# Optimization experiments

Measured on AMD Instinct MI355X. Metric: run time of the kernel, lower is better.

Reference implementation:

```python
import jax, jax.numpy as jnp
import numpy as np

EPS = 1e-12      # F.normalize eps
BN_EPS = 1e-5    # BatchNorm1d eps


def _l2norm(x):
    # x: (B, E, S); normalize over channel dim E (torch F.normalize default dim=1)
    n = jnp.sqrt(jnp.sum(x * x, axis=1, keepdims=True))
    return x / jnp.maximum(n, EPS)


def _conv1x1(w, b, x):
    # 1x1 Conv1d: w (O, E), b (O,), x (B, S, E) -> (B, O, S)
    return jnp.einsum('oe,bse->bos', w, x) + b[None, :, None]


def _batchnorm(x, g, b):
    # train-mode BatchNorm1d on (B, F): biased batch stats over dim 0
    m = jnp.mean(x, axis=0)
    v = jnp.var(x, axis=0)
    return (x - m) * jax.lax.rsqrt(v + BN_EPS) * g + b


def _pairwise(X, Y, wx, bx, wy, by, g, be, mxw, mxb, myw, myb):
    # X: (B, Sx, e), Y: (B, Sy, e)
    Xn = _l2norm(_conv1x1(wx, bx, X))           # (B, E, Sx)
    Yn = _l2norm(_conv1x1(wy, by, Y))           # (B, E, Sy)
    S = jnp.einsum('bex,bey->bxy', Xn, Yn)       # (B, Sx, Sy)
    B, Sx, Sy = S.shape
    S = _batchnorm(S.reshape(B, Sx * Sy), g, be).reshape(B, Sx, Sy)
    potX = jnp.einsum('y,bxy->bx', mxw, S) + mxb  # margin_X: Conv1d(Sy,1,1)
    potY = jnp.einsum('x,bxy->by', myw, S) + myb  # margin_Y: Conv1d(Sx,1,1)
    return potX, potY


def _pairwise_self(X, wx, bx, wy, by, g, be, mxw, mxb):
    # Pairwise with Y=None: embed_X and embed_Y both applied to X; only X_poten returned
    Xn = _l2norm(_conv1x1(wx, bx, X))
    Yn = _l2norm(_conv1x1(wy, by, X))
    S = jnp.einsum('bex,bey->bxy', Xn, Yn)
    B, Sx, Sy = S.shape
    S = _batchnorm(S.reshape(B, Sx * Sy), g, be).reshape(B, Sx, Sy)
    return jnp.einsum('y,bxy->bx', mxw, S) + mxb


def _unary(X, w1, b1, w2, b2):
    # Unary: conv1d e->e, relu, (dropout=identity in eval), conv1d e->1
    h = jax.nn.relu(_conv1x1(w1, b1, X))         # (B, E, S)
    return jnp.einsum('e,bes->bs', w2, h) + b2


def _forward(utils, un_w1, un_b1, un_w2, un_b2,
             sp_wx, sp_bx, sp_wy, sp_by, sp_g, sp_b, sp_mxw, sp_mxb,
             pw_wx, pw_bx, pw_wy, pw_by, pw_g, pw_b, pw_mxw, pw_mxb, pw_myw, pw_myb,
             red_w):
    # utils: (3, B, S, e)
    unp = jax.vmap(_unary)(utils, un_w1, un_b1, un_w2, un_b2)                    # (3, B, S)
    sfp = jax.vmap(_pairwise_self)(utils, sp_wx, sp_bx, sp_wy, sp_by,
                                   sp_g, sp_b, sp_mxw, sp_mxb)                   # (3, B, S)
    # pairwise pairs in combinations order: (0,1), (0,2), (1,2)
    idx_i = jnp.array([0, 0, 1])
    idx_j = jnp.array([1, 2, 2])
    pX, pY = jax.vmap(_pairwise)(utils[idx_i], utils[idx_j],
                                 pw_wx, pw_bx, pw_wy, pw_by, pw_g, pw_b,
                                 pw_mxw, pw_mxb, pw_myw, pw_myb)                 # (3, B, S) each
    pots = [
        [unp[0], sfp[0], pX[0], pX[1]],   # util 0: ij of (0,1), ij of (0,2)
        [unp[1], sfp[1], pY[0], pX[2]],   # util 1: ji of (0,1), ij of (1,2)
        [unp[2], sfp[2], pY[1], pY[2]],   # util 2: ji of (0,2), ji of (1,2)
    ]
    outs = []
    for i in range(3):
        P = jnp.stack(pots[i], axis=1)                 # (B, 4, S)
        red = jnp.einsum('k,bks->bs', red_w[i], P)     # Conv1d(4,1,1,bias=False)
        attn = jax.nn.softmax(red, axis=1)             # softmax over spatial dim
        outs.append(jnp.einsum('bse,bs->be', utils[i], attn))  # bmm(utils^T, attn)
    return jnp.stack(outs, axis=0)                     # (3, B, e)


def setup_inputs() -> dict:
    key = jax.random.key(0)
    ks = iter(jax.random.split(key, 32))
    def rn(shape, scale=0.05):
        return jax.random.normal(next(ks), shape, dtype=jnp.float32) * scale
    e, S, B, NU, NP = 128, 1024, 32, 3, 3
    F = S * S
    return dict(
        utils=rn((NU, B, S, e), 1.0),
        un_w1=rn((NU, e, e)), un_b1=rn((NU, e)), un_w2=rn((NU, e)), un_b2=rn((NU,)),
        sp_wx=rn((NU, e, e)), sp_bx=rn((NU, e)), sp_wy=rn((NU, e, e)), sp_by=rn((NU, e)),
        sp_g=jnp.ones((NU, F), jnp.float32), sp_b=jnp.zeros((NU, F), jnp.float32),
        sp_mxw=rn((NU, S)), sp_mxb=rn((NU,)),
        pw_wx=rn((NP, e, e)), pw_bx=rn((NP, e)), pw_wy=rn((NP, e, e)), pw_by=rn((NP, e)),
        pw_g=jnp.ones((NP, F), jnp.float32), pw_b=jnp.zeros((NP, F), jnp.float32),
        pw_mxw=rn((NP, S)), pw_mxb=rn((NP,)), pw_myw=rn((NP, S)), pw_myb=rn((NP,)),
        red_w=rn((NU, 4)),
    )


def reference(utils, un_w1, un_b1, un_w2, un_b2,
              sp_wx, sp_bx, sp_wy, sp_by, sp_g, sp_b, sp_mxw, sp_mxb,
              pw_wx, pw_bx, pw_wy, pw_by, pw_g, pw_b, pw_mxw, pw_mxb, pw_myw, pw_myb,
              red_w):
    return _forward(utils, un_w1, un_b1, un_w2, un_b2,
                    sp_wx, sp_bx, sp_wy, sp_by, sp_g, sp_b, sp_mxw, sp_mxb,
                    pw_wx, pw_bx, pw_wy, pw_by, pw_g, pw_b, pw_mxw, pw_mxb, pw_myw, pw_myb,
                    red_w)
```

## Files before the change

### kernel.cpp

```cpp
#include <hip/hip_runtime.h>
#include <math.h>

constexpr int EE = 128;
constexpr int NS = 1024;
constexpr int NB = 32;
constexpr size_t BSE = (size_t)NB * NS * EE;

typedef __attribute__((ext_vector_type(4))) float f32x4;
typedef __attribute__((ext_vector_type(8))) short s16x8;
typedef __attribute__((ext_vector_type(4))) short s16x4;
typedef __attribute__((ext_vector_type(8))) __bf16 bf16v8;

__device__ __forceinline__ f32x4 mfma16(s16x8 a, s16x8 b, f32x4 c) {
  return __builtin_amdgcn_mfma_f32_16x16x32_bf16(
      __builtin_bit_cast(bf16v8, a), __builtin_bit_cast(bf16v8, b), c, 0, 0, 0);
}

__device__ __forceinline__ unsigned short f2bf(float f) {
  unsigned u = __builtin_bit_cast(unsigned, f);
  u += 0x7FFFu + ((u >> 16) & 1u);
  return (unsigned short)(u >> 16);
}
__device__ __forceinline__ float bf2f(unsigned short h) {
  unsigned u = ((unsigned)h) << 16;
  return __builtin_bit_cast(float, u);
}

__device__ __forceinline__ int swz(int b)  { return b ^ (((b >> 8) & 7) << 4); }
__device__ __forceinline__ int swz7(int b) { return b ^ (((b >> 7) & 7) << 4); }

__device__ __forceinline__ void gl_lds16(const void* gptr, void* lptr) {
  auto g = (const __attribute__((address_space(1))) unsigned int*)gptr;
  auto l = (__attribute__((address_space(3))) unsigned int*)lptr;
  __builtin_amdgcn_global_load_lds(g, l, 16, 0, 0);
}

__device__ __forceinline__ void stage32k(const char* gsrc, char* ldst, int wv, int lane) {
#pragma unroll
  for (int c = 0; c < 8; ++c) {
    int uoff = c*4096 + wv*1024;
    gl_lds16(gsrc + swz(uoff + lane*16), ldst + uoff);
  }
}

__device__ __forceinline__ void stage_half(const char* tile, char* ldst, int kh, int wv, int lane) {
#pragma unroll
  for (int c = 0; c < 4; ++c) {
    int uoff = c*4096 + wv*1024;
    int sa = swz7(uoff + lane*16);
    gl_lds16(tile + (sa >> 7)*256 + kh*128 + (sa & 127), ldst + uoff);
  }
}

constexpr size_t EMB_OFF   = 0;
constexpr size_t UNP_OFF   = EMB_OFF + 12ull * BSE * 2;
constexpr size_t RB_OFF    = UNP_OFF + 3ull * NB * NS * 4;
constexpr size_t CX_OFF    = RB_OFF + 6ull * NS * NS * 2;
constexpr size_t POTX_OFF  = CX_OFF + 6ull * NS * 4;
constexpr size_t PYP_OFF   = POTX_OFF + 6ull * NB * NS * 4;
constexpr size_t CY_OFF    = PYP_OFF + 3ull * NB * 8 * NS * 4;
constexpr size_t CXP_OFF   = CY_OFF + 6ull * NS * 4;
constexpr size_t CYP_OFF   = CXP_OFF + 6ull * 8 * NS * 4;

__global__ __launch_bounds__(256, 2) void embed_kernel(
    const float* __restrict__ utils,
    const float* __restrict__ un_w1, const float* __restrict__ un_b1,
    const float* __restrict__ un_w2, const float* __restrict__ un_b2,
    const float* __restrict__ sp_wx, const float* __restrict__ sp_bx,
    const float* __restrict__ sp_wy, const float* __restrict__ sp_by,
    const float* __restrict__ pw_wx, const float* __restrict__ pw_bx,
    const float* __restrict__ pw_wy, const float* __restrict__ pw_by,
    unsigned short* __restrict__ emb, float* __restrict__ unp)
{
  const int u  = blockIdx.x >> 9;
  const int pt = blockIdx.x & 511;

  __shared__ short lA[64*128];
  __shared__ short lB[128*128];
  __shared__ float redbuf[64];

  const int t = threadIdx.x;
  {
    const char* src = (const char*)(utils + (size_t)u*BSE + (size_t)pt*64*EE);
#pragma unroll
    for (int c = 0; c < 8; ++c) {
      int off = c*4096 + t*16;
      float4 v = *(const float4*)(src + off);
      s16x4 h;
      h.x = (short)f2bf(v.x); h.y = (short)f2bf(v.y);
      h.z = (short)f2bf(v.z); h.w = (short)f2bf(v.w);
      *(s16x4*)((char*)lA + swz(off >> 1)) = h;
    }
  }

  const int lane = t & 63, wv = t >> 6;
  const int wrE = wv & 1, wcE = wv >> 1;
  const int cL = lane & 15, r4 = (lane >> 4) * 4, k8 = (lane >> 4) * 8;

  for (int m = 0; m < 5; ++m) {
    const float* W; const float* bias;
    unsigned short* dst = nullptr;
    int mode;
    if (m == 0)      { W = un_w1 + u*EE*EE; bias = un_b1 + u*EE; mode = 0; }
    else if (m == 1) { W = sp_wx + u*EE*EE; bias = sp_bx + u*EE; dst = emb + (size_t)(2*u)*BSE;   mode = 1; }
    else if (m == 2) { W = sp_wy + u*EE*EE; bias = sp_by + u*EE; dst = emb + (size_t)(2*u+1)*BSE; mode = 1; }
    else {
      int q, side;
      if (u == 0)      { q = (m == 3) ? 0 : 1; side = 0; }
      else if (u == 1) { if (m == 3) { q = 0; side = 1; } else { q = 2; side = 0; } }
      else             { q = (m == 3) ? 1 : 2; side = 1; }
      W    = (side == 0 ? pw_wx : pw_wy) + q*EE*EE;
      bias = (side == 0 ? pw_bx : pw_by) + q*EE;
      dst  = emb + (size_t)(2*(3+q)+side)*BSE;
      mode = 1;
    }

    __syncthreads();
    {
      const char* wsrc = (const char*)W;
#pragma unroll
      for (int c = 0; c < 16; ++c) {
        int off = c*4096 + t*16;
        float4 v = *(const float4*)(wsrc + off);
        s16x4 h;
        h.x = (short)f2bf(v.x); h.y = (short)f2bf(v.y);
        h.z = (short)f2bf(v.z); h.w = (short)f2bf(v.w);
        *(s16x4*)((char*)lB + swz(off >> 1)) = h;
      }
    }
    __syncthreads();

    f32x4 acc[2][4];
#pragma unroll
    for (int i = 0; i < 2; ++i)
#pragma unroll
      for (int j = 0; j < 4; ++j) acc[i][j] = f32x4{0.f, 0.f, 0.f, 0.f};

#pragma unroll
    for (int kk = 0; kk < 4; ++kk) {
      s16x8 av[2], bv[4];
#pragma unroll
      for (int i = 0; i < 2; ++i) {
        int row = wrE*32 + i*16 + cL;
        av[i] = *(const s16x8*)((const char*)lA + swz(row*256 + kk*64 + k8*2));
      }
#pragma unroll
      for (int j = 0; j < 4; ++j) {
        int row = wcE*64 + j*16 + cL;
        bv[j] = *(const s16x8*)((const char*)lB + swz(row*256 + kk*64 + k8*2));
      }
#pragma unroll
      for (int i = 0; i < 2; ++i)
#pragma unroll
        for (int j = 0; j < 4; ++j)
          acc[i][j] = mfma16(av[i], bv[j], acc[i][j]);
    }

    if (mode == 0) {
      const float* w2 = un_w2 + u*EE;
      float s[2][4];
#pragma unroll
      for (int i = 0; i < 2; ++i)
#pragma unroll
        for (int r = 0; r < 4; ++r) s[i][r] = 0.f;
#pragma unroll
      for (int i = 0; i < 2; ++i) {
#pragma unroll
        for (int j = 0; j < 4; ++j) {
          int o = wcE*64 + j*16 + cL;
          float bv2 = bias[o], w2v = w2[o];
#pragma unroll
          for (int r = 0; r < 4; ++r) {
            float v = acc[i][j][r] + bv2;
            v = v > 0.f ? v : 0.f;
            s[i][r] += v * w2v;
          }
        }
      }
#pragma unroll
      for (int msk = 1; msk < 16; msk <<= 1)
#pragma unroll
        for (int i = 0; i < 2; ++i)
#pragma unroll
          for (int r = 0; r < 4; ++r)
            s[i][r] += __shfl_xor(s[i][r], msk, 64);
      if (t < 64) redbuf[t] = 0.f;
      __syncthreads();
      if (cL == 0) {
#pragma unroll
        for (int i = 0; i < 2; ++i)
#pragma unroll
          for (int r = 0; r < 4; ++r)
            atomicAdd(&redbuf[wrE*32 + i*16 + r4 + r], s[i][r]);
      }
      __syncthreads();
      if (t < 64) unp[(size_t)u*NB*NS + (size_t)pt*64 + t] = redbuf[t] + un_b2[u];
    } else {
      float nrm[2][4];
#pragma unroll
      for (int i = 0; i < 2; ++i)
#pragma unroll
        for (int r = 0; r < 4; ++r) nrm[i][r] = 0.f;
#pragma unroll
      for (int i = 0; i < 2; ++i) {
#pragma unroll
        for (int j = 0; j < 4; ++j) {
          int o = wcE*64 + j*16 + cL;
          float bv2 = bias[o];
#pragma unroll
          for (int r = 0; r < 4; ++r) {
            acc[i][j][r] += bv2;
            nrm[i][r] += acc[i][j][r] * acc[i][j][r];
          }
        }
      }
#pragma unroll
      for (int msk = 1; msk < 16; msk <<= 1)
#pragma unroll
        for (int i = 0; i < 2; ++i)
#pragma unroll
          for (int r = 0; r < 4; ++r)
            nrm[i][r] += __shfl_xor(nrm[i][r], msk, 64);
      if (t < 64) redbuf[t] = 0.f;
      __syncthreads();
      if (cL == 0) {
#pragma unroll
        for (int i = 0; i < 2; ++i)
#pragma unroll
          for (int r = 0; r < 4; ++r)
            atomicAdd(&redbuf[wrE*32 + i*16 + r4 + r], nrm[i][r]);
      }
      __syncthreads();
#pragma unroll
      for (int i = 0; i < 2; ++i) {
#pragma unroll
        for (int r = 0; r < 4; ++r) {
          float n = redbuf[wrE*32 + i*16 + r4 + r];
          float sc = 1.f / fmaxf(sqrtf(n), 1e-12f);
          size_t pbase = ((size_t)pt*64 + wrE*32 + i*16 + r4 + r) * EE;
#pragma unroll
          for (int j = 0; j < 4; ++j) {
            int o = wcE*64 + j*16 + cL;
            dst[pbase + o] = f2bf(acc[i][j][r] * sc);
          }
        }
      }
    }
  }
}

__global__ __launch_bounds__(256, 2) void pass1_kernel(
    const unsigned short* __restrict__ emb,
    const float* __restrict__ sp_g, const float* __restrict__ sp_b,
    const float* __restrict__ sp_mxw,
    const float* __restrict__ pw_g, const float* __restrict__ pw_b,
    const float* __restrict__ pw_mxw, const float* __restrict__ pw_myw,
    unsigned short* __restrict__ Rb, float* __restrict__ cXpart,
    float* __restrict__ cYpart)
{
  const int bid = blockIdx.x;
  const int p = bid >> 6, xt = (bid >> 3) & 7, yt = bid & 7;
  const char* Xe = (const char*)(emb + (size_t)(2*p)*BSE + (size_t)xt*128*EE);
  const char* Ye = (const char*)(emb + (size_t)(2*p+1)*BSE + (size_t)yt*128*EE);
  __shared__ char lds[65536];
  __shared__ float cxbuf[128];
  __shared__ float cybuf[128];
  const int t = threadIdx.x, lane = t & 63, wv = t >> 6;
  const int wr = wv >> 1, wc = wv & 1, cL = lane & 15, r4 = (lane >> 4) * 4;
  const int q16 = (lane >> 4) * 16;

  f32x4 sS[4][4], sQ[4][4], acc[4][4];
#pragma unroll
  for (int i = 0; i < 4; ++i)
#pragma unroll
    for (int j = 0; j < 4; ++j) { sS[i][j] = f32x4{0.f,0.f,0.f,0.f}; sQ[i][j] = f32x4{0.f,0.f,0.f,0.f}; }

  stage_half(Xe, lds, 0, wv, lane);
  stage_half(Ye, lds + 16384, 0, wv, lane);
  if (t < 128) { cxbuf[t] = 0.f; cybuf[t] = 0.f; }
  __syncthreads();

  for (int s = 0; s < 2*NB; ++s) {
    const int cur = s & 1;
    const char* buf = lds + cur * 32768;
    if (s + 1 < 2*NB) {
      const int b1 = (s + 1) >> 1, kh1 = (s + 1) & 1;
      char* nb = lds + (cur ^ 1) * 32768;
      stage_half(Xe + (size_t)b1*NS*EE*2, nb, kh1, wv, lane);
      stage_half(Ye + (size_t)b1*NS*EE*2, nb + 16384, kh1, wv, lane);
    }
    if ((s & 1) == 0) {
#pragma unroll
      for (int i = 0; i < 4; ++i)
#pragma unroll
        for (int j = 0; j < 4; ++j) acc[i][j] = f32x4{0.f,0.f,0.f,0.f};
    }
#pragma unroll
    for (int kk2 = 0; kk2 < 2; ++kk2) {
      s16x8 av[4], bv[4];
#pragma unroll
      for (int i = 0; i < 4; ++i) {
        int row = wr*64 + i*16 + cL;
        av[i] = *(const s16x8*)(buf + swz7(row*128 + kk2*64 + q16));
      }
#pragma unroll
      for (int j = 0; j < 4; ++j) {
        int row = wc*64 + j*16 + cL;
        bv[j] = *(const s16x8*)(buf + 16384 + swz7(row*128 + kk2*64 + q16));
      }
#pragma unroll
      for (int i = 0; i < 4; ++i)
#pragma unroll
        for (int j = 0; j < 4; ++j)
          acc[i][j] = mfma16(av[i], bv[j], acc[i][j]);
    }
    if (s & 1) {
#pragma unroll
      for (int i = 0; i < 4; ++i)
#pragma unroll
        for (int j = 0; j < 4; ++j) {
          sS[i][j] += acc[i][j];
          sQ[i][j] += acc[i][j] * acc[i][j];
        }
    }
    __syncthreads();
  }

  const float* gp  = (p < 3) ? (sp_g + (size_t)p*NS*NS) : (pw_g + (size_t)(p-3)*NS*NS);
  const float* bbp = (p < 3) ? (sp_b + (size_t)p*NS*NS) : (pw_b + (size_t)(p-3)*NS*NS);
  const float* mxw = (p < 3) ? (sp_mxw + p*NS) : (pw_mxw + (p-3)*NS);
  const float* myw = (p < 3) ? nullptr : (pw_myw + (p-3)*NS);
  unsigned short* Rp = Rb + (size_t)p*NS*NS;
  const float inv = 1.f / 32.f;

  float mxl[4];
#pragma unroll
  for (int j = 0; j < 4; ++j) mxl[j] = mxw[yt*128 + wc*64 + j*16 + cL];
  float mywr[4][4];
  if (myw) {
#pragma unroll
    for (int i = 0; i < 4; ++i)
#pragma unroll
      for (int r = 0; r < 4; ++r)
        mywr[i][r] = myw[xt*128 + wr*64 + i*16 + r4 + r];
  }

  float py[4] = {0.f, 0.f, 0.f, 0.f};
#pragma unroll
  for (int i = 0; i < 4; ++i) {
#pragma unroll
    for (int r = 0; r < 4; ++r) {
      const size_t rowoff = (size_t)(xt*128 + wr*64 + i*16 + r4 + r)*NS + yt*128;
      float cxv = 0.f;
#pragma unroll
      for (int j = 0; j < 4; ++j) {
        int c = wc*64 + j*16 + cL;
        float mean = sS[i][j][r] * inv;
        float var  = sQ[i][j][r] * inv - mean * mean;
        float rstd = rsqrtf(var + 1e-5f);
        unsigned short rh = f2bf(gp[rowoff + c] * rstd);
        Rp[rowoff + c] = rh;
        float ct = bbp[rowoff + c] - bf2f(rh) * mean;
        cxv += mxl[j] * ct;
        if (myw) py[j] += mywr[i][r] * ct;
      }
      cxv += __shfl_xor(cxv, 1, 64);
      cxv += __shfl_xor(cxv, 2, 64);
      cxv += __shfl_xor(cxv, 4, 64);
      cxv += __shfl_xor(cxv, 8, 64);
      if (cL == 0) atomicAdd(&cxbuf[wr*64 + i*16 + r4 + r], cxv);
    }
  }
  if (myw) {
#pragma unroll
    for (int j = 0; j < 4; ++j) {
      py[j] += __shfl_xor(py[j], 16, 64);
      py[j] += __shfl_xor(py[j], 32, 64);
    }
    if ((lane >> 4) == 0) {
#pragma unroll
      for (int j = 0; j < 4; ++j)
        atomicAdd(&cybuf[wc*64 + j*16 + cL], py[j]);
    }
  }
  __syncthreads();
  if (t < 128) cXpart[((size_t)p*8 + yt)*NS + xt*128 + t] = cxbuf[t];
  if (myw && t < 128) cYpart[((size_t)(p-3)*8 + xt)*NS + yt*128 + t] = cybuf[t];
}

__global__ void cfin_kernel(
    const float* __restrict__ cXpart, const float* __restrict__ cYpart,
    const float* __restrict__ sp_mxb, const float* __restrict__ pw_mxb,
    float* __restrict__ cX, float* __restrict__ cY)
{
  const int blk = blockIdx.x;
  const int p = blk >> 2;
  const int x = ((blk & 3) << 8) + threadIdx.x;
  float a = 0.f;
#pragma unroll
  for (int yt = 0; yt < 8; ++yt) a += cXpart[((size_t)p*8 + yt)*NS + x];
  cX[p*NS + x] = a + (p < 3 ? sp_mxb[p] : pw_mxb[p-3]);
  if (p >= 3) {
    float b = 0.f;
#pragma unroll
    for (int xt = 0; xt < 8; ++xt) b += cYpart[((size_t)(p-3)*8 + xt)*NS + x];
    cY[p*NS + x] = b;
  }
}

__global__ __launch_bounds__(256, 2) void pass2_kernel(
    const unsigned short* __restrict__ emb, const unsigned short* __restrict__ Rb,
    const float* __restrict__ sp_mxw, const float* __restrict__ pw_mxw,
    const float* __restrict__ pw_myw,
    float* __restrict__ potX, float* __restrict__ potYpart)
{
  const int bid = blockIdx.x;
  const int p = bid >> 8, b = (bid >> 3) & 31, xt = bid & 7;
  const char* Ae = (const char*)(emb + (size_t)(2*p)*BSE + ((size_t)b*NS + (size_t)xt*128)*EE);
  const char* Be = (const char*)(emb + (size_t)(2*p+1)*BSE + (size_t)b*NS*EE);
  const unsigned short* Rp = Rb + (size_t)p*NS*NS;
  const float* mxw = (p < 3) ? (sp_mxw + p*NS) : (pw_mxw + (p-3)*NS);
  const float* myw = (p < 3) ? nullptr : (pw_myw + (p-3)*NS);
  __shared__ char lA[32768];
  __shared__ char lB[32768];
  __shared__ float pxbuf[128];
  __shared__ float pybuf[1024];
  const int t = threadIdx.x, lane = t & 63, wv = t >> 6;
  const int wr = wv >> 1, wc = wv & 1, cL = lane & 15, r4 = (lane >> 4) * 4, k8 = (lane >> 4) * 8;

  stage32k(Ae, lA, wv, lane);
  stage32k(Be, lB, wv, lane);
  if (t < 128) pxbuf[t] = 0.f;
#pragma unroll
  for (int k = 0; k < 4; ++k) pybuf[t + k*256] = 0.f;
  __syncthreads();

  float px[4][4];
#pragma unroll
  for (int i = 0; i < 4; ++i)
#pragma unroll
    for (int r = 0; r < 4; ++r) px[i][r] = 0.f;
  float mywv[4][4];
  if (myw) {
#pragma unroll
    for (int i = 0; i < 4; ++i)
#pragma unroll
      for (int r = 0; r < 4; ++r)
        mywv[i][r] = myw[xt*128 + wr*64 + i*16 + r4 + r];
  }

  for (int yt = 0; yt < 8; ++yt) {
    f32x4 acc[4][4];
#pragma unroll
    for (int i = 0; i < 4; ++i)
#pragma unroll
      for (int j = 0; j < 4; ++j) acc[i][j] = f32x4{0.f,0.f,0.f,0.f};
#pragma unroll
    for (int kk = 0; kk < 4; ++kk) {
      s16x8 av[4], bv[4];
#pragma unroll
      for (int i = 0; i < 4; ++i) {
        int row = wr*64 + i*16 + cL;
        av[i] = *(const s16x8*)(lA + swz(row*256 + kk*64 + k8*2));
      }
#pragma unroll
      for (int j = 0; j < 4; ++j) {
        int row = wc*64 + j*16 + cL;
        bv[j] = *(const s16x8*)(lB + swz(row*256 + kk*64 + k8*2));
      }
#pragma unroll
      for (int i = 0; i < 4; ++i)
#pragma unroll
        for (int j = 0; j < 4; ++j)
          acc[i][j] = mfma16(av[i], bv[j], acc[i][j]);
    }
    __syncthreads();

    float mxl[4];
#pragma unroll
    for (int j = 0; j < 4; ++j) mxl[j] = mxw[yt*128 + wc*64 + j*16 + cL];

    if (myw) {
      float py[4] = {0.f, 0.f, 0.f, 0.f};
#pragma unroll
      for (int i = 0; i < 4; ++i) {
#pragma unroll
        for (int r = 0; r < 4; ++r) {
          const unsigned short* Rr = Rp + (size_t)(xt*128 + wr*64 + i*16 + r4 + r)*NS + yt*128;
          float pxa = 0.f;
#pragma unroll
          for (int j = 0; j < 4; ++j) {
            float Rv = bf2f(Rr[wc*64 + j*16 + cL]);
            float tt = Rv * acc[i][j][r];
            pxa += mxl[j] * tt;
            py[j] += mywv[i][r] * tt;
          }
          px[i][r] += pxa;
        }
      }
#pragma unroll
      for (int j = 0; j < 4; ++j) {
        py[j] += __shfl_xor(py[j], 16, 64);
        py[j] += __shfl_xor(py[j], 32, 64);
      }
      if ((lane >> 4) == 0) {
#pragma unroll
        for (int j = 0; j < 4; ++j)
          atomicAdd(&pybuf[yt*128 + wc*64 + j*16 + cL], py[j]);
      }
    } else {
#pragma unroll
      for (int i = 0; i < 4; ++i) {
#pragma unroll
        for (int r = 0; r < 4; ++r) {
          const unsigned short* Rr = Rp + (size_t)(xt*128 + wr*64 + i*16 + r4 + r)*NS + yt*128;
          float pxa = 0.f;
#pragma unroll
          for (int j = 0; j < 4; ++j) {
            float Rv = bf2f(Rr[wc*64 + j*16 + cL]);
            pxa += mxl[j] * (Rv * acc[i][j][r]);
          }
          px[i][r] += pxa;
        }
      }
    }

    if (yt < 7)
      stage32k(Be + (size_t)(yt+1)*32768, lB, wv, lane);
    __syncthreads();
  }

#pragma unroll
  for (int msk = 1; msk < 16; msk <<= 1)
#pragma unroll
    for (int i = 0; i < 4; ++i)
#pragma unroll
      for (int r = 0; r < 4; ++r)
        px[i][r] += __shfl_xor(px[i][r], msk, 64);
  if (cL == 0) {
#pragma unroll
    for (int i = 0; i < 4; ++i)
#pragma unroll
      for (int r = 0; r < 4; ++r)
        atomicAdd(&pxbuf[wr*64 + i*16 + r4 + r], px[i][r]);
  }
  __syncthreads();
  if (t < 128) potX[((size_t)p*NB + b)*NS + (size_t)xt*128 + t] = pxbuf[t];

  if (myw) {
    const size_t base = ((size_t)((p-3)*NB + b) * 8 + xt) * NS;
#pragma unroll
    for (int k = 0; k < 4; ++k)
      potYpart[base + t + k*256] = pybuf[t + k*256];
  }
}

__global__ __launch_bounds__(256, 4) void final_kernel(
    const float* __restrict__ utils, const float* __restrict__ unp,
    const float* __restrict__ potX, const float* __restrict__ pyp,
    const float* __restrict__ cX, const float* __restrict__ cY,
    const float* __restrict__ pw_myb, const float* __restrict__ red_w,
    float* __restrict__ out)
{
  const int u = blockIdx.x >> 5, b = blockIdx.x & 31, t = threadIdx.x;
  const int lane = t & 63, wv = t >> 6;
  __shared__ float wts[1024];
  __shared__ float redA[4], redB[4];
  __shared__ float comb[128];
  const float* unpp  = unp  + ((size_t)u*NB + b)*NS;
  const float* selfX = potX + ((size_t)u*NB + b)*NS;
  const float* cXu   = cX + u*NS;
  const float rw0 = red_w[u*4+0], rw1 = red_w[u*4+1], rw2 = red_w[u*4+2], rw3 = red_w[u*4+3];

  int ty2, ty3; const float *x2 = nullptr, *x3 = nullptr, *c2, *c3;
  const float *y2 = nullptr, *y3 = nullptr; float a2 = 0.f, a3 = 0.f;
  if (u == 0) {
    ty2 = 0; x2 = potX + ((size_t)3*NB + b)*NS; c2 = cX + 3*NS;
    ty3 = 0; x3 = potX + ((size_t)4*NB + b)*NS; c3 = cX + 4*NS;
  } else if (u == 1) {
    ty2 = 1; y2 = pyp + ((size_t)(0*NB + b) * 8) * NS; c2 = cY + 3*NS; a2 = pw_myb[0];
    ty3 = 0; x3 = potX + ((size_t)5*NB + b)*NS; c3 = cX + 5*NS;
  } else {
    ty2 = 1; y2 = pyp + ((size_t)(1*NB + b) * 8) * NS; c2 = cY + 4*NS; a2 = pw_myb[1];
    ty3 = 1; y3 = pyp + ((size_t)(2*NB + b) * 8) * NS; c3 = cY + 5*NS; a3 = pw_myb[2];
  }
  float rv[4]; float lmax = -3.4e38f;
#pragma unroll
  for (int k = 0; k < 4; ++k) {
    int s = t*4 + k;
    float t2, t3;
    if (ty2 == 0) t2 = x2[s] + c2[s];
    else {
      float a = 0.f;
#pragma unroll
      for (int q = 0; q < 8; ++q) a += y2[(size_t)q*NS + s];
      t2 = a + c2[s] + a2;
    }
    if (ty3 == 0) t3 = x3[s] + c3[s];
    else {
      float a = 0.f;
#pragma unroll
      for (int q = 0; q < 8; ++q) a += y3[(size_t)q*NS + s];
      t3 = a + c3[s] + a3;
    }
    float v = rw0*unpp[s] + rw1*(selfX[s] + cXu[s]) + rw2*t2 + rw3*t3;
    rv[k] = v; lmax = fmaxf(lmax, v);
  }
#pragma unroll
  for (int msk = 1; msk < 64; msk <<= 1) lmax = fmaxf(lmax, __shfl_xor(lmax, msk, 64));
  if (lane == 0) redA[wv] = lmax;
  __syncthreads();
  const float gmax = fmaxf(fmaxf(redA[0], redA[1]), fmaxf(redA[2], redA[3]));
  float lsum = 0.f;
#pragma unroll
  for (int k = 0; k < 4; ++k) {
    float e2 = __expf(rv[k] - gmax);
    wts[t*4 + k] = e2; lsum += e2;
  }
#pragma unroll
  for (int msk = 1; msk < 64; msk <<= 1) lsum += __shfl_xor(lsum, msk, 64);
  if (lane == 0) redB[wv] = lsum;
  __syncthreads();
  const float inv = 1.f / (redB[0] + redB[1] + redB[2] + redB[3]);
  const int e = t & 127, half = t >> 7;
  const float* ub = utils + (size_t)u*BSE + (size_t)b*NS*EE;
  float acc = 0.f;
  const int s0 = half * 512;
#pragma unroll 8
  for (int s = s0; s < s0 + 512; ++s)
    acc += ub[(size_t)s*EE + e] * wts[s];
  if (half) comb[e] = acc;
  __syncthreads();
  if (!half) out[((size_t)u*NB + b)*EE + e] = (acc + comb[e]) * inv;
}

extern "C" void kernel_launch(void* const* d_in, const int* in_sizes, int n_in,
                              void* d_out, int out_size, void* d_ws, size_t ws_size,
                              hipStream_t stream)
{
  (void)in_sizes; (void)n_in; (void)out_size; (void)ws_size;
  const float* utils  = (const float*)d_in[0];
  const float* un_w1  = (const float*)d_in[1];
  const float* un_b1  = (const float*)d_in[2];
  const float* un_w2  = (const float*)d_in[3];
  const float* un_b2  = (const float*)d_in[4];
  const float* sp_wx  = (const float*)d_in[5];
  const float* sp_bx  = (const float*)d_in[6];
  const float* sp_wy  = (const float*)d_in[7];
  const float* sp_by  = (const float*)d_in[8];
  const float* sp_g   = (const float*)d_in[9];
  const float* sp_b   = (const float*)d_in[10];
  const float* sp_mxw = (const float*)d_in[11];
  const float* sp_mxb = (const float*)d_in[12];
  const float* pw_wx  = (const float*)d_in[13];
  const float* pw_bx  = (const float*)d_in[14];
  const float* pw_wy  = (const float*)d_in[15];
  const float* pw_by  = (const float*)d_in[16];
  const float* pw_g   = (const float*)d_in[17];
  const float* pw_b   = (const float*)d_in[18];
  const float* pw_mxw = (const float*)d_in[19];
  const float* pw_mxb = (const float*)d_in[20];
  const float* pw_myw = (const float*)d_in[21];
  const float* pw_myb = (const float*)d_in[22];
  const float* red_w  = (const float*)d_in[23];
  float* out = (float*)d_out;
  char* ws = (char*)d_ws;

  unsigned short* embp  = (unsigned short*)(ws + EMB_OFF);
  float* unpp           = (float*)(ws + UNP_OFF);
  unsigned short* Rbp   = (unsigned short*)(ws + RB_OFF);
  float* cXp            = (float*)(ws + CX_OFF);
  float* potXp          = (float*)(ws + POTX_OFF);
  float* pypp           = (float*)(ws + PYP_OFF);
  float* cYp            = (float*)(ws + CY_OFF);
  float* cXpartp        = (float*)(ws + CXP_OFF);
  float* cYpartp        = (float*)(ws + CYP_OFF);

  embed_kernel<<<dim3(1536), dim3(256), 0, stream>>>(
      utils, un_w1, un_b1, un_w2, un_b2, sp_wx, sp_bx, sp_wy, sp_by,
      pw_wx, pw_bx, pw_wy, pw_by, embp, unpp);
  pass1_kernel<<<dim3(384), dim3(256), 0, stream>>>(
      embp, sp_g, sp_b, sp_mxw, pw_g, pw_b, pw_mxw, pw_myw,
      Rbp, cXpartp, cYpartp);
  cfin_kernel<<<dim3(24), dim3(256), 0, stream>>>(
      cXpartp, cYpartp, sp_mxb, pw_mxb, cXp, cYp);
  pass2_kernel<<<dim3(1536), dim3(256), 0, stream>>>(
      embp, Rbp, sp_mxw, pw_mxw, pw_myw, potXp, pypp);
  final_kernel<<<dim3(96), dim3(256), 0, stream>>>(
      utils, unpp, potXp, pypp, cXp, cYp, pw_myb, red_w, out);
}
```

Before: 270.8 us.

## Pre-convert weights to bf16 and split final weighted sum across more blocks

Adds a prep kernel that converts all fifteen 128x128 weight matrices to bf16 once, so embed blocks stage them with async LDS loads instead of each of the 1536 blocks reconverting fp32 weights. It also raises embed occupancy to 3 blocks per CU. The final kernel is split into a softmax kernel, a 768-block weighted-sum kernel over 128-row chunks, and a small reduction kernel. The old final kernel ran only 96 blocks, each streaming 512 KB of utils, so this spreads that work across the GPU at the cost of two extra launches and partial-sum traffic.

```diff
diff --git a/kernel.cpp b/kernel.cpp
--- a/kernel.cpp
+++ b/kernel.cpp
@@ -61,15 +61,36 @@
 constexpr size_t CY_OFF    = PYP_OFF + 3ull * NB * 8 * NS * 4;
 constexpr size_t CXP_OFF   = CY_OFF + 6ull * NS * 4;
 constexpr size_t CYP_OFF   = CXP_OFF + 6ull * 8 * NS * 4;
-
-__global__ __launch_bounds__(256, 2) void embed_kernel(
-    const float* __restrict__ utils,
-    const float* __restrict__ un_w1, const float* __restrict__ un_b1,
-    const float* __restrict__ un_w2, const float* __restrict__ un_b2,
-    const float* __restrict__ sp_wx, const float* __restrict__ sp_bx,
-    const float* __restrict__ sp_wy, const float* __restrict__ sp_by,
-    const float* __restrict__ pw_wx, const float* __restrict__ pw_bx,
-    const float* __restrict__ pw_wy, const float* __restrict__ pw_by,
+constexpr size_t WBF_OFF   = CYP_OFF + 3ull * 8 * NS * 4;
+constexpr size_t WTS_OFF   = WBF_OFF + 15ull * EE * EE * 2;
+constexpr size_t PART_OFF  = WTS_OFF + 3ull * NB * NS * 4;
+
+__global__ void wprep_kernel(
+    const float* __restrict__ un_w1, const float* __restrict__ sp_wx,
+    const float* __restrict__ sp_wy, const float* __restrict__ pw_wx,
+    const float* __restrict__ pw_wy, unsigned short* __restrict__ wbf)
+{
+  const int i = (blockIdx.x * 256 + threadIdx.x) * 4;
+  const int m15 = i >> 14, off = i & 16383;
+  const float* src;
+  if (m15 < 3)       src = un_w1 + (size_t)m15 * 16384;
+  else if (m15 < 6)  src = sp_wx + (size_t)(m15 - 3) * 16384;
+  else if (m15 < 9)  src = sp_wy + (size_t)(m15 - 6) * 16384;
+  else if (m15 < 12) src = pw_wx + (size_t)(m15 - 9) * 16384;
+  else               src = pw_wy + (size_t)(m15 - 12) * 16384;
+  float4 v = *(const float4*)(src + off);
+  s16x4 h;
+  h.x = (short)f2bf(v.x); h.y = (short)f2bf(v.y);
+  h.z = (short)f2bf(v.z); h.w = (short)f2bf(v.w);
+  *(s16x4*)(wbf + i) = h;
+}
+
+__global__ __launch_bounds__(256, 3) void embed_kernel(
+    const float* __restrict__ utils, const unsigned short* __restrict__ wbf,
+    const float* __restrict__ un_b1, const float* __restrict__ un_w2,
+    const float* __restrict__ un_b2,
+    const float* __restrict__ sp_bx, const float* __restrict__ sp_by,
+    const float* __restrict__ pw_bx, const float* __restrict__ pw_by,
     unsigned short* __restrict__ emb, float* __restrict__ unp)
 {
   const int u  = blockIdx.x >> 9;
@@ -98,36 +119,25 @@
   const int cL = lane & 15, r4 = (lane >> 4) * 4, k8 = (lane >> 4) * 8;
 
   for (int m = 0; m < 5; ++m) {
-    const float* W; const float* bias;
+    int wid; const float* bias;
     unsigned short* dst = nullptr;
     int mode;
-    if (m == 0)      { W = un_w1 + u*EE*EE; bias = un_b1 + u*EE; mode = 0; }
-    else if (m == 1) { W = sp_wx + u*EE*EE; bias = sp_bx + u*EE; dst = emb + (size_t)(2*u)*BSE;   mode = 1; }
-    else if (m == 2) { W = sp_wy + u*EE*EE; bias = sp_by + u*EE; dst = emb + (size_t)(2*u+1)*BSE; mode = 1; }
+    if (m == 0)      { wid = u;     bias = un_b1 + u*EE; mode = 0; }
+    else if (m == 1) { wid = 3 + u; bias = sp_bx + u*EE; dst = emb + (size_t)(2*u)*BSE;   mode = 1; }
+    else if (m == 2) { wid = 6 + u; bias = sp_by + u*EE; dst = emb + (size_t)(2*u+1)*BSE; mode = 1; }
     else {
       int q, side;
       if (u == 0)      { q = (m == 3) ? 0 : 1; side = 0; }
       else if (u == 1) { if (m == 3) { q = 0; side = 1; } else { q = 2; side = 0; } }
       else             { q = (m == 3) ? 1 : 2; side = 1; }
-      W    = (side == 0 ? pw_wx : pw_wy) + q*EE*EE;
+      wid  = (side == 0 ? 9 : 12) + q;
       bias = (side == 0 ? pw_bx : pw_by) + q*EE;
       dst  = emb + (size_t)(2*(3+q)+side)*BSE;
       mode = 1;
     }
 
     __syncthreads();
-    {
-      const char* wsrc = (const char*)W;
-#pragma unroll
-      for (int c = 0; c < 16; ++c) {
-        int off = c*4096 + t*16;
-        float4 v = *(const float4*)(wsrc + off);
-        s16x4 h;
-        h.x = (short)f2bf(v.x); h.y = (short)f2bf(v.y);
-        h.z = (short)f2bf(v.z); h.w = (short)f2bf(v.w);
-        *(s16x4*)((char*)lB + swz(off >> 1)) = h;
-      }
-    }
+    stage32k((const char*)wbf + (size_t)wid * 32768, (char*)lB, wv, lane);
     __syncthreads();
 
     f32x4 acc[2][4];
@@ -555,18 +565,16 @@
   }
 }
 
-__global__ __launch_bounds__(256, 4) void final_kernel(
-    const float* __restrict__ utils, const float* __restrict__ unp,
+__global__ __launch_bounds__(256, 4) void softmax_kernel(
+    const float* __restrict__ unp,
     const float* __restrict__ potX, const float* __restrict__ pyp,
     const float* __restrict__ cX, const float* __restrict__ cY,
     const float* __restrict__ pw_myb, const float* __restrict__ red_w,
-    float* __restrict__ out)
+    float* __restrict__ wtsn)
 {
   const int u = blockIdx.x >> 5, b = blockIdx.x & 31, t = threadIdx.x;
   const int lane = t & 63, wv = t >> 6;
-  __shared__ float wts[1024];
   __shared__ float redA[4], redB[4];
-  __shared__ float comb[128];
   const float* unpp  = unp  + ((size_t)u*NB + b)*NS;
   const float* selfX = potX + ((size_t)u*NB + b)*NS;
   const float* cXu   = cX + u*NS;
@@ -611,27 +619,50 @@
   if (lane == 0) redA[wv] = lmax;
   __syncthreads();
   const float gmax = fmaxf(fmaxf(redA[0], redA[1]), fmaxf(redA[2], redA[3]));
-  float lsum = 0.f;
+  float e2v[4]; float lsum = 0.f;
 #pragma unroll
   for (int k = 0; k < 4; ++k) {
-    float e2 = __expf(rv[k] - gmax);
-    wts[t*4 + k] = e2; lsum += e2;
+    e2v[k] = __expf(rv[k] - gmax);
+    lsum += e2v[k];
   }
 #pragma unroll
   for (int msk = 1; msk < 64; msk <<= 1) lsum += __shfl_xor(lsum, msk, 64);
   if (lane == 0) redB[wv] = lsum;
   __syncthreads();
   const float inv = 1.f / (redB[0] + redB[1] + redB[2] + redB[3]);
-  const int e = t & 127, half = t >> 7;
-  const float* ub = utils + (size_t)u*BSE + (size_t)b*NS*EE;
+  float4 w4 = {e2v[0]*inv, e2v[1]*inv, e2v[2]*inv, e2v[3]*inv};
+  *(float4*)(wtsn + ((size_t)u*NB + b)*NS + t*4) = w4;
+}
+
+__global__ __launch_bounds__(256, 8) void bmm_kernel(
+    const float* __restrict__ utils, const float* __restrict__ wtsn,
+    float* __restrict__ part)
+{
+  const int blk = blockIdx.x;
+  const int ch = blk & 7, ub = blk >> 3;
+  const int b = ub & 31, u = ub >> 5;
+  const int t = threadIdx.x, e = t & 127, half = t >> 7;
+  __shared__ float comb[128];
+  const float* w  = wtsn + (size_t)ub*NS + ch*128;
+  const float* up = utils + (size_t)u*BSE + ((size_t)b*NS + ch*128)*EE;
   float acc = 0.f;
-  const int s0 = half * 512;
+  const int s0 = half * 64;
 #pragma unroll 8
-  for (int s = s0; s < s0 + 512; ++s)
-    acc += ub[(size_t)s*EE + e] * wts[s];
+  for (int s = s0; s < s0 + 64; ++s)
+    acc += up[(size_t)s*EE + e] * w[s];
   if (half) comb[e] = acc;
   __syncthreads();
-  if (!half) out[((size_t)u*NB + b)*EE + e] = (acc + comb[e]) * inv;
+  if (!half) part[(size_t)blk*128 + e] = acc + comb[e];
+}
+
+__global__ void fred_kernel(const float* __restrict__ part, float* __restrict__ out)
+{
+  const int idx = blockIdx.x * 256 + threadIdx.x;
+  const int e = idx & 127, ub = idx >> 7;
+  float a = 0.f;
+#pragma unroll
+  for (int ch = 0; ch < 8; ++ch) a += part[((size_t)ub*8 + ch)*128 + e];
+  out[idx] = a;
 }
 
 extern "C" void kernel_launch(void* const* d_in, const int* in_sizes, int n_in,
@@ -675,10 +706,14 @@
   float* cYp            = (float*)(ws + CY_OFF);
   float* cXpartp        = (float*)(ws + CXP_OFF);
   float* cYpartp        = (float*)(ws + CYP_OFF);
-
+  unsigned short* wbfp  = (unsigned short*)(ws + WBF_OFF);
+  float* wtsp           = (float*)(ws + WTS_OFF);
+  float* partp          = (float*)(ws + PART_OFF);
+
+  wprep_kernel<<<dim3(240), dim3(256), 0, stream>>>(
+      un_w1, sp_wx, sp_wy, pw_wx, pw_wy, wbfp);
   embed_kernel<<<dim3(1536), dim3(256), 0, stream>>>(
-      utils, un_w1, un_b1, un_w2, un_b2, sp_wx, sp_bx, sp_wy, sp_by,
-      pw_wx, pw_bx, pw_wy, pw_by, embp, unpp);
+      utils, wbfp, un_b1, un_w2, un_b2, sp_bx, sp_by, pw_bx, pw_by, embp, unpp);
   pass1_kernel<<<dim3(384), dim3(256), 0, stream>>>(
       embp, sp_g, sp_b, sp_mxw, pw_g, pw_b, pw_mxw, pw_myw,
       Rbp, cXpartp, cYpartp);
@@ -686,6 +721,9 @@
       cXpartp, cYpartp, sp_mxb, pw_mxb, cXp, cYp);
   pass2_kernel<<<dim3(1536), dim3(256), 0, stream>>>(
       embp, Rbp, sp_mxw, pw_mxw, pw_myw, potXp, pypp);
-  final_kernel<<<dim3(96), dim3(256), 0, stream>>>(
-      utils, unpp, potXp, pypp, cXp, cYp, pw_myb, red_w, out);
-}
+  softmax_kernel<<<dim3(96), dim3(256), 0, stream>>>(
+      unpp, potXp, pypp, cXp, cYp, pw_myb, red_w, wtsp);
+  bmm_kernel<<<dim3(768), dim3(256), 0, stream>>>(
+      utils, wtsp, partp);
+  fred_kernel<<<dim3(48), dim3(256), 0, stream>>>(partp, out);
+}
```

New measurement: 259.4 us (median of 3 runs). 1.04x faster.
